# Performance work log

Hardware: AMD Instinct MI355X
Metric: run time of the kernel (lower is better)

The kernel has to match this reference:

```python
import jax, jax.numpy as jnp
import numpy as np

N_EMBED = 384
BLOCK_SIZE = 256
HEAD_SIZE = 64
B, T = 256, 256


def setup_inputs() -> dict:
    key = jax.random.key(0)
    k1, k2, k3, k4 = jax.random.split(key, 4)
    x = jax.random.normal(k1, (B, T, N_EMBED), dtype=jnp.float32)
    Wq = jax.random.normal(k2, (N_EMBED, HEAD_SIZE), dtype=jnp.float32) * (N_EMBED ** -0.5)
    Wk = jax.random.normal(k3, (N_EMBED, HEAD_SIZE), dtype=jnp.float32) * (N_EMBED ** -0.5)
    Wv = jax.random.normal(k4, (N_EMBED, HEAD_SIZE), dtype=jnp.float32) * (N_EMBED ** -0.5)
    return {"x": x, "Wq": Wq, "Wk": Wk, "Wv": Wv}


def reference(x, Wq, Wk, Wv):
    Bb, Tt, C = x.shape
    q = jnp.einsum("btc,ch->bth", x, Wq)
    k = jnp.einsum("btc,ch->bth", x, Wk)
    v = jnp.einsum("btc,ch->bth", x, Wv)
    # NOTE: original scales by C**-0.5 where C = n_embed (384), not head_size
    scale = jnp.asarray(C, x.dtype) ** -0.5
    wei = jnp.einsum("bqh,bkh->bqk", q, k) * scale  # [B, T, T]
    causal = jnp.tril(jnp.ones((Tt, Tt), dtype=bool))
    wei = jnp.where(causal, wei, -jnp.inf)
    wei = jax.nn.softmax(wei, axis=-1)
    out = jnp.einsum("bqk,bkh->bqh", wei, v)
    return out
```

## Files before the change

kernel.cpp:

```cpp
#include <hip/hip_runtime.h>
#include <hip/hip_bf16.h>
#include <math.h>

#define BB   256
#define TT   256
#define CIN  384
#define HS   64

#define QSCL ((float)(0.051031036307982884 * 1.4426950408889634))

typedef __attribute__((ext_vector_type(8))) short short8;
typedef __attribute__((ext_vector_type(4))) float floatx4;

__device__ inline short bf16bits(float f) {
    union { __hip_bfloat16 h; short s; } u;
    u.h = __float2bfloat16(f);
    return u.s;
}

__device__ inline short8 cvt8(const float4& f0, const float4& f1) {
    union { __hip_bfloat162 h[4]; short8 s8; } u;
    u.h[0] = __float22bfloat162_rn(make_float2(f0.x, f0.y));
    u.h[1] = __float22bfloat162_rn(make_float2(f0.z, f0.w));
    u.h[2] = __float22bfloat162_rn(make_float2(f1.x, f1.y));
    u.h[3] = __float22bfloat162_rn(make_float2(f1.z, f1.w));
    return u.s8;
}

__global__ __launch_bounds__(256) void prep_wtp(
    const float* __restrict__ Wq, const float* __restrict__ Wk,
    const float* __restrict__ Wv, short* __restrict__ WtP)
{
    const int idx  = blockIdx.x * 256 + threadIdx.x;
    const int j    = idx & 7;
    const int quad = (idx >> 3) & 3;
    const int l15  = (idx >> 5) & 15;
    int X          = idx >> 9;
    const int nt   = X % 6;  X /= 6;
    const int ks   = X & 1;  X >>= 1;
    const int s    = X % 6;  X /= 6;
    const int wn   = X;

    const int n  = wn * 96 + nt * 16 + l15;
    const int kk = s * 64 + ks * 32 + quad * 8 + j;
    const float* W = (n < 64) ? Wq : (n < 128) ? Wk : Wv;
    WtP[idx] = bf16bits(W[kk * 64 + (n & 63)]);
}

__global__ __launch_bounds__(1024, 4) void fused_head(
    const float* __restrict__ x, const short* __restrict__ WtP,
    float* __restrict__ out)
{
    __shared__ short smem[59392];

    const int tid  = threadIdx.x;
    const int b    = blockIdx.x;
    const int lane = tid & 63;
    const int w    = tid >> 6;
    const int l15  = lane & 15;
    const int quad = lane >> 4;
    const int kq   = quad * 8;
    const int crow = quad * 4;

    const float* xb = x + (size_t)b * 256 * 384;
    const int laneoff = l15 * 32 + kq;

    floatx4 acc[12] = {};

    const float* xr = xb + (size_t)(w * 16 + l15) * 384 + kq;

    float4 c00 = *(const float4*)(xr + 0);
    float4 c01 = *(const float4*)(xr + 4);
    float4 c10 = *(const float4*)(xr + 32);
    float4 c11 = *(const float4*)(xr + 36);

#pragma unroll
    for (int s = 0; s < 6; ++s) {
        float4 n00, n01, n10, n11;
        if (s < 5) {
            n00 = *(const float4*)(xr + (s + 1) * 64 + 0);
            n01 = *(const float4*)(xr + (s + 1) * 64 + 4);
            n10 = *(const float4*)(xr + (s + 1) * 64 + 32);
            n11 = *(const float4*)(xr + (s + 1) * 64 + 36);
        }
        const short8 af0 = cvt8(c00, c01);
        const short8 af1 = cvt8(c10, c11);
#pragma unroll
        for (int ks = 0; ks < 2; ++ks) {
            const short8 af = ks ? af1 : af0;
#pragma unroll
            for (int h = 0; h < 2; ++h) {
                short8 bf[6];
#pragma unroll
                for (int nt = 0; nt < 6; ++nt)
                    bf[nt] = *(const short8*)
                        &WtP[((((h * 6 + s) * 2 + ks) * 6 + nt) << 9) + laneoff];
#pragma unroll
                for (int nt = 0; nt < 6; ++nt)
                    acc[h * 6 + nt] = __builtin_amdgcn_mfma_f32_16x16x32_bf16(
                        af, bf[nt], acc[h * 6 + nt], 0, 0, 0);
            }
        }
        if (s < 5) { c00 = n00; c01 = n01; c10 = n10; c11 = n11; }
    }

    short* qP = smem;
    short* kP = smem + 16384;
    short* vP = smem + 32768;
    short* Ps = smem + 49152;

#pragma unroll
    for (int j = 0; j < 12; ++j) {
#pragma unroll
        for (int r = 0; r < 4; ++r) {
            const int n  = j * 16 + l15;
            const int mr = crow + r;
            const float av = acc[j][r];
            if (j < 4) {
                const int h = j >> 1;
                qP[((w * 2 + h) * 16 + mr) * 32 + ((n & 31) >> 3) * 8 + (n & 7)]
                    = bf16bits(av * QSCL);
            } else if (j < 8) {
                const int h = (j - 4) >> 1;
                kP[((w * 2 + h) * 16 + mr) * 32 + (((n - 64) & 31) >> 3) * 8 + (n & 7)]
                    = bf16bits(av);
            } else {
                const int nb = j - 8;
                const int kk = (w & 1) * 16 + mr;
                vP[(((w >> 1) * 4 + nb) * 16 + l15) * 32 + kk] = bf16bits(av);
            }
        }
    }
    __syncthreads();

    {
        const int g  = w;
        const int r0 = g * 16;

        const short8 aq0 = *(const short8*)&qP[((g * 2 + 0) * 16 + l15) * 32 + kq];
        const short8 aq1 = *(const short8*)&qP[((g * 2 + 1) * 16 + l15) * 32 + kq];

        float lsum[4] = {0.f, 0.f, 0.f, 0.f};
        floatx4 O[4] = {};

        const int nch = (r0 + 47) >> 5;
        for (int c = 0; c < nch; ++c) {
            const int cb = c * 32;

            floatx4 st[2];
#pragma unroll
            for (int t = 0; t < 2; ++t) {
                const short8 b0 = *(const short8*)
                    &kP[(((c * 2 + t) * 2 + 0) * 16 + l15) * 32 + kq];
                const short8 b1 = *(const short8*)
                    &kP[(((c * 2 + t) * 2 + 1) * 16 + l15) * 32 + kq];
                floatx4 z = {};
                z = __builtin_amdgcn_mfma_f32_16x16x32_bf16(aq0, b0, z, 0, 0, 0);
                z = __builtin_amdgcn_mfma_f32_16x16x32_bf16(aq1, b1, z, 0, 0, 0);
                st[t] = z;
            }

#pragma unroll
            for (int t = 0; t < 2; ++t)
#pragma unroll
                for (int r = 0; r < 4; ++r) {
                    const int key  = cb + t * 16 + l15;
                    const int qrow = r0 + crow + r;
                    float p = __builtin_amdgcn_exp2f(st[t][r]);
                    p = (key <= qrow) ? p : 0.f;
                    lsum[r] += p;
                    Ps[w * 640 + (crow + r) * 40 + t * 16 + l15] = bf16bits(p);
                }

            asm volatile("s_waitcnt lgkmcnt(0)" ::: "memory");

            const short8 pa = *(const short8*)&Ps[w * 640 + l15 * 40 + kq];
#pragma unroll
            for (int n = 0; n < 4; ++n) {
                const short8 bv = *(const short8*)
                    &vP[((c * 4 + n) * 16 + l15) * 32 + kq];
                O[n] = __builtin_amdgcn_mfma_f32_16x16x32_bf16(pa, bv, O[n], 0, 0, 0);
            }
        }

#pragma unroll
        for (int off = 1; off < 16; off <<= 1)
#pragma unroll
            for (int r = 0; r < 4; ++r)
                lsum[r] += __shfl_xor(lsum[r], off, 16);

        float inv[4];
#pragma unroll
        for (int r = 0; r < 4; ++r) inv[r] = 1.f / lsum[r];
#pragma unroll
        for (int n = 0; n < 4; ++n)
#pragma unroll
            for (int r = 0; r < 4; ++r)
                out[(size_t)(b * 256 + r0 + crow + r) * 64 + n * 16 + l15]
                    = O[n][r] * inv[r];
    }
}

extern "C" void kernel_launch(void* const* d_in, const int* in_sizes, int n_in,
                              void* d_out, int out_size, void* d_ws, size_t ws_size,
                              hipStream_t stream)
{
    const float* x  = (const float*)d_in[0];
    const float* Wq = (const float*)d_in[1];
    const float* Wk = (const float*)d_in[2];
    const float* Wv = (const float*)d_in[3];
    float* out = (float*)d_out;

    short* WtP = (short*)d_ws;

    prep_wtp<<<(192 * 384) / 256, 256, 0, stream>>>(Wq, Wk, Wv, WtP);
    fused_head<<<BB, 1024, 0, stream>>>(x, WtP, out);
}
```

Baseline: 181.1 us.

## Split fused head kernel into separate QKV GEMM and load-balanced attention kernels

```diff
diff --git a/kernel.cpp b/kernel.cpp
--- a/kernel.cpp
+++ b/kernel.cpp
@@ -11,6 +11,7 @@
 
 typedef __attribute__((ext_vector_type(8))) short short8;
 typedef __attribute__((ext_vector_type(4))) float floatx4;
+typedef __attribute__((ext_vector_type(4))) float fx4;
 
 __device__ inline short bf16bits(float f) {
     union { __hip_bfloat16 h; short s; } u;
@@ -18,13 +19,17 @@
     return u.s;
 }
 
-__device__ inline short8 cvt8(const float4& f0, const float4& f1) {
+__device__ inline short8 cvt8(const fx4& f0, const fx4& f1) {
     union { __hip_bfloat162 h[4]; short8 s8; } u;
     u.h[0] = __float22bfloat162_rn(make_float2(f0.x, f0.y));
     u.h[1] = __float22bfloat162_rn(make_float2(f0.z, f0.w));
     u.h[2] = __float22bfloat162_rn(make_float2(f1.x, f1.y));
     u.h[3] = __float22bfloat162_rn(make_float2(f1.z, f1.w));
     return u.s8;
+}
+
+__device__ inline fx4 ntload4(const float* p) {
+    return __builtin_nontemporal_load((const fx4*)p);
 }
 
 __global__ __launch_bounds__(256) void prep_wtp(
@@ -47,98 +52,106 @@
     WtP[idx] = bf16bits(W[kk * 64 + (n & 63)]);
 }
 
-__global__ __launch_bounds__(1024, 4) void fused_head(
+__global__ __launch_bounds__(512, 2) void qkv_gemm(
     const float* __restrict__ x, const short* __restrict__ WtP,
-    float* __restrict__ out)
-{
-    __shared__ short smem[59392];
-
+    short* __restrict__ qF, short* __restrict__ kF, short* __restrict__ vF)
+{
     const int tid  = threadIdx.x;
-    const int b    = blockIdx.x;
     const int lane = tid & 63;
     const int w    = tid >> 6;
     const int l15  = lane & 15;
     const int quad = lane >> 4;
     const int kq   = quad * 8;
     const int crow = quad * 4;
-
-    const float* xb = x + (size_t)b * 256 * 384;
+    const int job  = blockIdx.x * 8 + w;
     const int laneoff = l15 * 32 + kq;
 
+    const float* xr = x + (size_t)(job * 16 + l15) * 384 + kq;
+
     floatx4 acc[12] = {};
 
-    const float* xr = xb + (size_t)(w * 16 + l15) * 384 + kq;
-
-    float4 c00 = *(const float4*)(xr + 0);
-    float4 c01 = *(const float4*)(xr + 4);
-    float4 c10 = *(const float4*)(xr + 32);
-    float4 c11 = *(const float4*)(xr + 36);
+    fx4 c00 = ntload4(xr + 0);
+    fx4 c01 = ntload4(xr + 4);
+    fx4 c10 = ntload4(xr + 32);
+    fx4 c11 = ntload4(xr + 36);
 
 #pragma unroll
     for (int s = 0; s < 6; ++s) {
-        float4 n00, n01, n10, n11;
-        if (s < 5) {
-            n00 = *(const float4*)(xr + (s + 1) * 64 + 0);
-            n01 = *(const float4*)(xr + (s + 1) * 64 + 4);
-            n10 = *(const float4*)(xr + (s + 1) * 64 + 32);
-            n11 = *(const float4*)(xr + (s + 1) * 64 + 36);
-        }
         const short8 af0 = cvt8(c00, c01);
         const short8 af1 = cvt8(c10, c11);
-#pragma unroll
-        for (int ks = 0; ks < 2; ++ks) {
+        if (s < 5) {
+            c00 = ntload4(xr + (s + 1) * 64 + 0);
+            c01 = ntload4(xr + (s + 1) * 64 + 4);
+            c10 = ntload4(xr + (s + 1) * 64 + 32);
+            c11 = ntload4(xr + (s + 1) * 64 + 36);
+        }
+#pragma unroll
+        for (int q = 0; q < 4; ++q) {
+            const int ks = q >> 1, h = q & 1;
+            short8 bb[6];
+#pragma unroll
+            for (int nt = 0; nt < 6; ++nt)
+                bb[nt] = *(const short8*)
+                    &WtP[((((h * 6 + s) * 2 + ks) * 6 + nt) << 9) + laneoff];
+            __builtin_amdgcn_sched_barrier(0);
             const short8 af = ks ? af1 : af0;
 #pragma unroll
-            for (int h = 0; h < 2; ++h) {
-                short8 bf[6];
-#pragma unroll
-                for (int nt = 0; nt < 6; ++nt)
-                    bf[nt] = *(const short8*)
-                        &WtP[((((h * 6 + s) * 2 + ks) * 6 + nt) << 9) + laneoff];
-#pragma unroll
-                for (int nt = 0; nt < 6; ++nt)
-                    acc[h * 6 + nt] = __builtin_amdgcn_mfma_f32_16x16x32_bf16(
-                        af, bf[nt], acc[h * 6 + nt], 0, 0, 0);
-            }
-        }
-        if (s < 5) { c00 = n00; c01 = n01; c10 = n10; c11 = n11; }
+            for (int nt = 0; nt < 6; ++nt)
+                acc[h * 6 + nt] = __builtin_amdgcn_mfma_f32_16x16x32_bf16(
+                    af, bb[nt], acc[h * 6 + nt], 0, 0, 0);
+        }
     }
 
-    short* qP = smem;
-    short* kP = smem + 16384;
-    short* vP = smem + 32768;
-    short* Ps = smem + 49152;
-
+    const int b = job >> 4;
+    const int g = job & 15;
 #pragma unroll
     for (int j = 0; j < 12; ++j) {
 #pragma unroll
         for (int r = 0; r < 4; ++r) {
-            const int n  = j * 16 + l15;
-            const int mr = crow + r;
             const float av = acc[j][r];
             if (j < 4) {
-                const int h = j >> 1;
-                qP[((w * 2 + h) * 16 + mr) * 32 + ((n & 31) >> 3) * 8 + (n & 7)]
+                qF[(((b * 16 + g) * 2 + (j >> 1)) << 9)
+                   + (crow + r) * 32 + (j & 1) * 16 + l15]
                     = bf16bits(av * QSCL);
             } else if (j < 8) {
-                const int h = (j - 4) >> 1;
-                kP[((w * 2 + h) * 16 + mr) * 32 + (((n - 64) & 31) >> 3) * 8 + (n & 7)]
+                kF[(((b * 16 + g) * 2 + ((j - 4) >> 1)) << 9)
+                   + (crow + r) * 32 + (j & 1) * 16 + l15]
                     = bf16bits(av);
             } else {
-                const int nb = j - 8;
-                const int kk = (w & 1) * 16 + mr;
-                vP[(((w >> 1) * 4 + nb) * 16 + l15) * 32 + kk] = bf16bits(av);
+                vF[(((b * 4 + (j - 8)) * 8 + (g >> 1)) << 9)
+                   + l15 * 32 + (g & 1) * 16 + crow + r]
+                    = bf16bits(av);
             }
         }
     }
-    __syncthreads();
-
-    {
-        const int g  = w;
+}
+
+__global__ __launch_bounds__(256, 4) void attn(
+    const short* __restrict__ qF, const short* __restrict__ kF,
+    const short* __restrict__ vF, float* __restrict__ out)
+{
+    __shared__ short Ps[4 * 16 * 40];
+
+    const int tid  = threadIdx.x;
+    const int lane = tid & 63;
+    const int wv   = tid >> 6;
+    const int l15  = lane & 15;
+    const int quad = lane >> 4;
+    const int kq   = quad * 8;
+    const int crow = quad * 4;
+
+    const int b = blockIdx.x >> 1;
+    const int p = (blockIdx.x & 1) * 4 + wv;
+
+#pragma unroll
+    for (int gi = 0; gi < 2; ++gi) {
+        const int g  = gi ? (15 - p) : p;
         const int r0 = g * 16;
 
-        const short8 aq0 = *(const short8*)&qP[((g * 2 + 0) * 16 + l15) * 32 + kq];
-        const short8 aq1 = *(const short8*)&qP[((g * 2 + 1) * 16 + l15) * 32 + kq];
+        const short8 aq0 = *(const short8*)
+            &qF[(((b * 16 + g) * 2 + 0) << 9) + l15 * 32 + kq];
+        const short8 aq1 = *(const short8*)
+            &qF[(((b * 16 + g) * 2 + 1) << 9) + l15 * 32 + kq];
 
         float lsum[4] = {0.f, 0.f, 0.f, 0.f};
         floatx4 O[4] = {};
@@ -151,9 +164,9 @@
 #pragma unroll
             for (int t = 0; t < 2; ++t) {
                 const short8 b0 = *(const short8*)
-                    &kP[(((c * 2 + t) * 2 + 0) * 16 + l15) * 32 + kq];
+                    &kF[(((b * 16 + (2 * c + t)) * 2 + 0) << 9) + l15 * 32 + kq];
                 const short8 b1 = *(const short8*)
-                    &kP[(((c * 2 + t) * 2 + 1) * 16 + l15) * 32 + kq];
+                    &kF[(((b * 16 + (2 * c + t)) * 2 + 1) << 9) + l15 * 32 + kq];
                 floatx4 z = {};
                 z = __builtin_amdgcn_mfma_f32_16x16x32_bf16(aq0, b0, z, 0, 0, 0);
                 z = __builtin_amdgcn_mfma_f32_16x16x32_bf16(aq1, b1, z, 0, 0, 0);
@@ -166,20 +179,20 @@
                 for (int r = 0; r < 4; ++r) {
                     const int key  = cb + t * 16 + l15;
                     const int qrow = r0 + crow + r;
-                    float p = __builtin_amdgcn_exp2f(st[t][r]);
-                    p = (key <= qrow) ? p : 0.f;
-                    lsum[r] += p;
-                    Ps[w * 640 + (crow + r) * 40 + t * 16 + l15] = bf16bits(p);
+                    float pp = __builtin_amdgcn_exp2f(st[t][r]);
+                    pp = (key <= qrow) ? pp : 0.f;
+                    lsum[r] += pp;
+                    Ps[wv * 640 + (crow + r) * 40 + t * 16 + l15] = bf16bits(pp);
                 }
 
             asm volatile("s_waitcnt lgkmcnt(0)" ::: "memory");
 
-            const short8 pa = *(const short8*)&Ps[w * 640 + l15 * 40 + kq];
-#pragma unroll
-            for (int n = 0; n < 4; ++n) {
+            const short8 pa = *(const short8*)&Ps[wv * 640 + l15 * 40 + kq];
+#pragma unroll
+            for (int nb = 0; nb < 4; ++nb) {
                 const short8 bv = *(const short8*)
-                    &vP[((c * 4 + n) * 16 + l15) * 32 + kq];
-                O[n] = __builtin_amdgcn_mfma_f32_16x16x32_bf16(pa, bv, O[n], 0, 0, 0);
+                    &vF[(((b * 4 + nb) * 8 + c) << 9) + l15 * 32 + kq];
+                O[nb] = __builtin_amdgcn_mfma_f32_16x16x32_bf16(pa, bv, O[nb], 0, 0, 0);
             }
         }
 
@@ -193,11 +206,11 @@
 #pragma unroll
         for (int r = 0; r < 4; ++r) inv[r] = 1.f / lsum[r];
 #pragma unroll
-        for (int n = 0; n < 4; ++n)
+        for (int nb = 0; nb < 4; ++nb)
 #pragma unroll
             for (int r = 0; r < 4; ++r)
-                out[(size_t)(b * 256 + r0 + crow + r) * 64 + n * 16 + l15]
-                    = O[n][r] * inv[r];
+                out[(size_t)(b * 256 + r0 + crow + r) * 64 + nb * 16 + l15]
+                    = O[nb][r] * inv[r];
     }
 }
 
@@ -212,7 +225,11 @@
     float* out = (float*)d_out;
 
     short* WtP = (short*)d_ws;
+    short* qF  = WtP + 73728;
+    short* kF  = qF + 4194304;
+    short* vF  = kF + 4194304;
 
     prep_wtp<<<(192 * 384) / 256, 256, 0, stream>>>(Wq, Wk, Wv, WtP);
-    fused_head<<<BB, 1024, 0, stream>>>(x, WtP, out);
-}
+    qkv_gemm<<<512, 512, 0, stream>>>(x, WtP, qF, kF, vF);
+    attn<<<512, 256, 0, stream>>>(qF, kF, vF, out);
+}
```

Result: slower. 198.2 us (+9.4%).
